# Kernel tuning notes

Hardware: AMD Instinct MI355X
Metric: run time of the kernel (lower is better)

## Reference

```python
import jax, jax.numpy as jnp
import numpy as np


def setup_inputs() -> dict:
    key = jax.random.key(0)
    k1, k2, k3 = jax.random.split(key, 3)
    n_sup, n_qry, d, n_classes = 512, 2097152, 64, 16
    support_features = jax.random.normal(k1, (n_sup, d), dtype=jnp.float32)
    query_features = jax.random.normal(k2, (n_qry, d), dtype=jnp.float32)
    support_labels = jnp.arange(n_sup, dtype=jnp.int64) % n_classes  # every class populated
    query_labels = jax.random.randint(k3, (n_qry,), 0, n_classes, dtype=jnp.int64)
    return {
        "support_features": support_features,
        "query_features": query_features,
        "support_labels": support_labels,
        "query_labels": query_labels,
        "n_classes": n_classes,
        "n_iter": 50,
        "beta": 5,
    }


def _sq_dists(q, q_sq, centroids):
    # squared Euclidean distances [Nq, C]; q_sq precomputed row norms of q
    return q_sq[:, None] - 2.0 * (q @ centroids.T) + jnp.sum(centroids * centroids, axis=-1)[None, :]


def reference(support_features, query_features, support_labels, query_labels, n_classes, n_iter, beta):
    dtype = support_features.dtype
    beta_f = jnp.asarray(beta, dtype)
    # per-class support sums/counts (hard assignments, fixed across iterations)
    oh = jax.nn.one_hot(support_labels, n_classes, dtype=dtype)        # [Ns, C]
    class_counts = jnp.sum(oh, axis=0)                                  # [C]
    sup_sum = oh.T @ support_features                                   # [C, d]
    centroids = sup_sum / class_counts[:, None]                         # class means init

    q_sq = jnp.sum(query_features * query_features, axis=-1)            # [Nq]

    def step(centroids, _):
        d2 = _sq_dists(query_features, q_sq, centroids)                 # [Nq, C]
        w = jax.nn.softmax(-beta_f * d2, axis=-1)                       # soft assignments
        num = sup_sum + w.T @ query_features                            # [C, d]
        den = class_counts + jnp.sum(w, axis=0)                         # [C]
        return num / den[:, None], None

    centroids, _ = jax.lax.scan(step, centroids, None, length=n_iter)

    d2 = _sq_dists(query_features, q_sq, centroids)
    pred = jnp.argmin(d2, axis=-1)
    acc = jnp.mean((pred == query_labels).astype(jnp.float32))
    return acc
```

## Files before the change

### kernel.cpp

```cpp
#include <hip/hip_runtime.h>
#include <stdint.h>

typedef short bf16x8 __attribute__((ext_vector_type(8)));
typedef float f32x4 __attribute__((ext_vector_type(4)));
typedef float f32x2 __attribute__((ext_vector_type(2)));
typedef uint32_t u32x4 __attribute__((ext_vector_type(4)));
typedef uint32_t u32x2 __attribute__((ext_vector_type(2)));
typedef int i32x2 __attribute__((ext_vector_type(2)));
typedef unsigned short u16;
typedef long long i64;

#define ITERS 50
#define BETA_F 5.0f

#define WS_SUPSUM 0
#define WS_COUNTS 1024
#define WS_CENT   1040
#define WS_CSQ    2064
#define WS_ACC    2080
#define WS_CORR   10400
#define WS_Q8_OFF 10432

__device__ __forceinline__ u16 f2bf(float x) {
  union { float f; uint32_t u; } v; v.f = x;
  uint32_t r = (v.u + 0x7FFFu + ((v.u >> 16) & 1u)) >> 16;
  return (u16)r;
}
__device__ __forceinline__ uint32_t fkey(float f) {
  union { float f; uint32_t u; } v; v.f = f;
  return (v.u & 0x80000000u) ? ~v.u : (v.u | 0x80000000u);
}
__device__ __forceinline__ uint32_t pk8(float a, float b, float c, float d) {
  int r = __builtin_amdgcn_cvt_pk_fp8_f32(a, b, 0, false);
  r = __builtin_amdgcn_cvt_pk_fp8_f32(c, d, r, true);
  return (uint32_t)r;
}
__device__ __forceinline__ i64 pack64(uint32_t lo, uint32_t hi) {
  return (i64)(((uint64_t)hi << 32) | (uint64_t)lo);
}
__device__ __forceinline__ void quant_hilo4(float v0, float v1, float v2, float v3,
                                            uint32_t& hi, uint32_t& lo, float& sq) {
  uint32_t h = pk8(v0, v1, v2, v3);
  float h0 = __builtin_amdgcn_cvt_f32_fp8((int)h, 0);
  float h1 = __builtin_amdgcn_cvt_f32_fp8((int)h, 1);
  float h2 = __builtin_amdgcn_cvt_f32_fp8((int)h, 2);
  float h3 = __builtin_amdgcn_cvt_f32_fp8((int)h, 3);
  uint32_t l = pk8(v0 - h0, v1 - h1, v2 - h2, v3 - h3);
  float c0 = h0 + __builtin_amdgcn_cvt_f32_fp8((int)l, 0);
  float c1 = h1 + __builtin_amdgcn_cvt_f32_fp8((int)l, 1);
  float c2 = h2 + __builtin_amdgcn_cvt_f32_fp8((int)l, 2);
  float c3 = h3 + __builtin_amdgcn_cvt_f32_fp8((int)l, 3);
  sq += c0 * c0 + c1 * c1 + c2 * c2 + c3 * c3;
  hi = h; lo = l;
}

__device__ __forceinline__ i32x2 ds_tr8(const uint8_t* p) {
#if defined(__has_builtin)
#if __has_builtin(__builtin_amdgcn_ds_read_tr8_b64)
#define HAVE_TR8 1
#endif
#endif
#ifdef HAVE_TR8
  typedef __attribute__((address_space(3))) i32x2 lds_i32x2;
  return __builtin_amdgcn_ds_read_tr8_b64((lds_i32x2*)p);
#else
  uint32_t off = (uint32_t)(uintptr_t)(__attribute__((address_space(3))) const void*)p;
  i32x2 r;
  asm volatile("ds_read_b64_tr_b8 %0, %1\n\ts_waitcnt lgkmcnt(0)"
               : "=v"(r) : "v"(off) : "memory");
  __builtin_amdgcn_sched_barrier(0);
  return r;
#endif
}

template <int CTRL>
__device__ __forceinline__ float dppf(float x) {
  int i = __builtin_bit_cast(int, x);
  int r = __builtin_amdgcn_update_dpp(i, i, CTRL, 0xF, 0xF, false);
  return __builtin_bit_cast(float, r);
}
template <int CTRL>
__device__ __forceinline__ uint32_t dppu(uint32_t x) {
  int r = __builtin_amdgcn_update_dpp((int)x, (int)x, CTRL, 0xF, 0xF, false);
  return (uint32_t)r;
}
__device__ __forceinline__ float rmax16(float x) {
  x = fmaxf(x, dppf<0xB1>(x));
  x = fmaxf(x, dppf<0x4E>(x));
  x = fmaxf(x, dppf<0x141>(x));
  x = fmaxf(x, dppf<0x140>(x));
  return x;
}
__device__ __forceinline__ float rsum16(float x) {
  x += dppf<0xB1>(x);
  x += dppf<0x4E>(x);
  x += dppf<0x141>(x);
  x += dppf<0x140>(x);
  return x;
}
__device__ __forceinline__ uint32_t rumax16(uint32_t x) {
  uint32_t t;
  t = dppu<0xB1>(x);  x = (t > x) ? t : x;
  t = dppu<0x4E>(x);  x = (t > x) ? t : x;
  t = dppu<0x141>(x); x = (t > x) ? t : x;
  t = dppu<0x140>(x); x = (t > x) ? t : x;
  return x;
}

__global__ __launch_bounds__(1024) void init_kernel(const float* __restrict__ sup,
                                                    const int* __restrict__ slab,
                                                    int NS, float* __restrict__ ws) {
  const int tid = threadIdx.x;
  const int c = tid >> 6, j = tid & 63;
  float s = 0.f; int cnt = 0;
  for (int i = 0; i < NS; ++i) {
    int lbl = slab[i];
    float v = sup[i * 64 + j];
    if (lbl == c) { s += v; cnt++; }
  }
  ws[WS_SUPSUM + tid] = s;
  if (j == 0) ws[WS_COUNTS + c] = (float)cnt;
  ws[WS_CENT + tid] = s / (float)cnt;
  for (int i = tid; i < 8 * 1040; i += 1024) ws[WS_ACC + i] = 0.f;
  if (tid == 0) ws[WS_CORR] = 0.f;
  __syncthreads();
  if (j == 0) {
    float sq = 0.f;
    for (int k = 0; k < 64; ++k) { float v = ws[WS_CENT + c * 64 + k]; sq += v * v; }
    ws[WS_CSQ + c] = sq;
  }
}

template <bool SRC_F8, bool WRC8>
__global__ __launch_bounds__(256, 4) void pass_kernel(const float* __restrict__ qf,
                                                      uint8_t* __restrict__ q8,
                                                      int NQ, float* __restrict__ ws) {
  __shared__ __attribute__((aligned(16))) uint8_t qt8[4][2048];
  __shared__ __attribute__((aligned(16))) uint8_t w8[4][16][32];
  __shared__ float redden[16];

  const int tid = threadIdx.x;
  const int lane = tid & 63;
  const int wv = tid >> 6;
  const int c = lane & 15;
  const int g = lane >> 4;

  const float* cent = ws + WS_CENT;
  const int cb = c * 64 + g * 8;
  uint32_t bh0a, bl0a, bh0b, bl0b, bh1a, bl1a, bh1b, bl1b;
  float csq = 0.f;
  quant_hilo4(cent[cb + 0], cent[cb + 1], cent[cb + 2], cent[cb + 3], bh0a, bl0a, csq);
  quant_hilo4(cent[cb + 4], cent[cb + 5], cent[cb + 6], cent[cb + 7], bh0b, bl0b, csq);
  quant_hilo4(cent[cb + 32], cent[cb + 33], cent[cb + 34], cent[cb + 35], bh1a, bl1a, csq);
  quant_hilo4(cent[cb + 36], cent[cb + 37], cent[cb + 38], cent[cb + 39], bh1b, bl1b, csq);
  csq += __shfl_xor(csq, 16);
  csq += __shfl_xor(csq, 32);
  const i64 bh0 = pack64(bh0a, bh0b), bl0 = pack64(bl0a, bl0b);
  const i64 bh1 = pack64(bh1a, bh1b), bl1 = pack64(bl1a, bl1b);
  const float kcn = -BETA_F * csq;

  f32x4 acc[4] = {};
  float denacc = 0.f;

  uint8_t* qtw = &qt8[wv][0];
  const uint8_t* trb = qtw + c + g * 128;
  uint8_t* w8w = &w8[wv][c][0];
  const int woff = (g >> 1) * 512 + (g & 1) * 8;

  const int wave_id = blockIdx.x * 4 + wv;
  const int nwaves = gridDim.x * 4;
  const int ntiles = NQ >> 5;

  auto LOADQ = [&](int tl, u32x2 (&da)[2], u32x2 (&db)[2]) {
    const int qb0 = tl << 5;
#pragma unroll
    for (int st = 0; st < 2; ++st) {
      const int q = qb0 + st * 16 + c;
      if (SRC_F8) {
        u32x4 v = *(const u32x4*)(q8 + (size_t)q * 64 + g * 16);
        da[st][0] = v[0]; da[st][1] = v[1];
        db[st][0] = v[2]; db[st][1] = v[3];
      } else {
        const float* qr = qf + (size_t)q * 64 + g * 8;
        f32x4 v0 = *(const f32x4*)(qr);
        f32x4 v1 = *(const f32x4*)(qr + 4);
        f32x4 v2 = *(const f32x4*)(qr + 32);
        f32x4 v3 = *(const f32x4*)(qr + 36);
        da[st][0] = pk8(v0[0], v0[1], v0[2], v0[3]);
        da[st][1] = pk8(v1[0], v1[1], v1[2], v1[3]);
        db[st][0] = pk8(v2[0], v2[1], v2[2], v2[3]);
        db[st][1] = pk8(v3[0], v3[1], v3[2], v3[3]);
        if (WRC8) {
          u32x4 o; o[0] = da[st][0]; o[1] = da[st][1]; o[2] = db[st][0]; o[3] = db[st][1];
          *(u32x4*)(q8 + (size_t)q * 64 + g * 16) = o;
        }
      }
    }
  };

  u32x2 qa[2] = {}, qb_[2] = {}, na_[2] = {}, nb_[2] = {};
  int tile = wave_id;
  if (tile < ntiles) LOADQ(tile, qa, qb_);
  for (; tile < ntiles; tile += nwaves) {
    if (tile + nwaves < ntiles) LOADQ(tile + nwaves, na_, nb_);
#pragma unroll
    for (int st = 0; st < 2; ++st) {
      const int row = st * 16 + c;
      *(u32x2*)(qtw + woff + row * 16) = qa[st];
      *(u32x2*)(qtw + woff + row * 16 + 1024) = qb_[st];
      const i64 a0 = __builtin_bit_cast(i64, qa[st]);
      const i64 a1 = __builtin_bit_cast(i64, qb_[st]);
      f32x4 sc4 = {};
      sc4 = __builtin_amdgcn_mfma_f32_16x16x32_fp8_fp8(a0, bh0, sc4, 0, 0, 0);
      sc4 = __builtin_amdgcn_mfma_f32_16x16x32_fp8_fp8(a0, bl0, sc4, 0, 0, 0);
      sc4 = __builtin_amdgcn_mfma_f32_16x16x32_fp8_fp8(a1, bh1, sc4, 0, 0, 0);
      sc4 = __builtin_amdgcn_mfma_f32_16x16x32_fp8_fp8(a1, bl1, sc4, 0, 0, 0);
      float wr[4];
#pragma unroll
      for (int r = 0; r < 4; ++r) {
        float sv = fmaf(sc4[r], 2.0f * BETA_F, kcn);
        float m = rmax16(sv);
        float e = __expf(sv - m);
        float s = rsum16(e);
        wr[r] = e * __builtin_amdgcn_rcpf(s);
      }
      uint32_t w32 = pk8(wr[0], wr[1], wr[2], wr[3]);
      *(uint32_t*)(w8w + st * 16 + g * 4) = w32;
      f32x2 d0 = __builtin_amdgcn_cvt_pk_f32_fp8((int)w32, false);
      f32x2 d1 = __builtin_amdgcn_cvt_pk_f32_fp8((int)w32, true);
      denacc += (d0[0] + d0[1]) + (d1[0] + d1[1]);
    }
    const i64 aw = *(const i64*)(w8w + g * 8);
#pragma unroll
    for (int nt = 0; nt < 4; ++nt) {
      i32x2 bq = ds_tr8(trb + nt * 512);
      acc[nt] = __builtin_amdgcn_mfma_f32_16x16x32_fp8_fp8(
          aw, __builtin_bit_cast(i64, bq), acc[nt], 0, 0, 0);
    }
#pragma unroll
    for (int st = 0; st < 2; ++st) { qa[st] = na_[st]; qb_[st] = nb_[st]; }
  }

  __syncthreads();
  float* red = (float*)&qt8[0][0];
  for (int i = tid; i < 1024; i += 256) red[i] = 0.f;
  if (tid < 16) redden[tid] = 0.f;
  __syncthreads();
#pragma unroll
  for (int nt = 0; nt < 4; ++nt)
#pragma unroll
    for (int r = 0; r < 4; ++r)
      atomicAdd(&red[(g * 4 + r) * 64 + nt * 16 + c], acc[nt][r]);
  atomicAdd(&redden[c], denacc);
  __syncthreads();
  float* accn = ws + WS_ACC + (size_t)(blockIdx.x & 7) * 1040;
  for (int i = tid; i < 1024; i += 256) atomicAdd(&accn[i], red[i]);
  if (tid < 16) atomicAdd(&accn[1024 + tid], redden[tid]);
}

__global__ __launch_bounds__(1024) void update_kernel(float* __restrict__ ws) {
  const int tid = threadIdx.x;
  const int c = tid >> 6;
  float num = ws[WS_SUPSUM + tid];
  float den = ws[WS_COUNTS + c];
#pragma unroll
  for (int rep = 0; rep < 8; ++rep) {
    num += ws[WS_ACC + rep * 1040 + tid];
    den += ws[WS_ACC + rep * 1040 + 1024 + c];
  }
  ws[WS_CENT + tid] = num / den;
  for (int i = tid; i < 8 * 1040; i += 1024) ws[WS_ACC + i] = 0.f;
  __syncthreads();
  if ((tid & 63) == 0) {
    float sq = 0.f;
    for (int k = 0; k < 64; ++k) { float v = ws[WS_CENT + c * 64 + k]; sq += v * v; }
    ws[WS_CSQ + c] = sq;
  }
}

__global__ __launch_bounds__(256, 4) void final_kernel(const float* __restrict__ qf,
                                                       const int* __restrict__ qlab,
                                                       int NQ, float* __restrict__ ws) {
  const int tid = threadIdx.x;
  const int lane = tid & 63;
  const int c = lane & 15;
  const int g = lane >> 4;

  const float* cent = ws + WS_CENT;
  bf16x8 bc0, bc1;
#pragma unroll
  for (int j = 0; j < 8; ++j) {
    bc0[j] = (short)f2bf(cent[c * 64 + g * 8 + j]);
    bc1[j] = (short)f2bf(cent[c * 64 + 32 + g * 8 + j]);
  }
  const float csq = ws[WS_CSQ + c];

  int cnt = 0;
  const int wave_id = blockIdx.x * 4 + (tid >> 6);
  const int nwaves = gridDim.x * 4;
  const int ntiles = NQ >> 4;

  for (int tile = wave_id; tile < ntiles; tile += nwaves) {
    const int qbase = tile << 4;
    const int q = qbase + c;
    const float* qrow = qf + (size_t)q * 64;
    bf16x8 a0, a1;
#pragma unroll
    for (int j = 0; j < 8; ++j) {
      a0[j] = (short)f2bf(qrow[g * 8 + j]);
      a1[j] = (short)f2bf(qrow[32 + g * 8 + j]);
    }
    f32x4 sc = (f32x4){0.f, 0.f, 0.f, 0.f};
    sc = __builtin_amdgcn_mfma_f32_16x16x32_bf16(a0, bc0, sc, 0, 0, 0);
    sc = __builtin_amdgcn_mfma_f32_16x16x32_bf16(a1, bc1, sc, 0, 0, 0);
#pragma unroll
    for (int r = 0; r < 4; ++r) {
      float val = 2.f * sc[r] - csq;
      uint32_t key = (fkey(val) & 0xFFFFFFF0u) | (uint32_t)(15 - c);
      key = rumax16(key);
      int pred = 15 - (int)(key & 15u);
      if (c == 0) cnt += (qlab[qbase + g * 4 + r] == pred) ? 1 : 0;
    }
  }
#pragma unroll
  for (int msk = 1; msk < 64; msk <<= 1) cnt += __shfl_xor(cnt, msk);
  if (lane == 0) atomicAdd(&ws[WS_CORR], (float)cnt);
}

__global__ void finalize_kernel(const float* __restrict__ ws, float* __restrict__ out, float inv) {
  out[0] = ws[WS_CORR] * inv;
}

extern "C" void kernel_launch(void* const* d_in, const int* in_sizes, int n_in,
                              void* d_out, int out_size, void* d_ws, size_t ws_size,
                              hipStream_t stream) {
  const float* sup = (const float*)d_in[0];
  const float* qf  = (const float*)d_in[1];
  const int* slab  = (const int*)d_in[2];
  const int* qlab  = (const int*)d_in[3];
  float* ws = (float*)d_ws;
  float* out = (float*)d_out;
  const int NS = in_sizes[0] / 64;
  const int NQ = in_sizes[1] / 64;
  uint8_t* q8 = (uint8_t*)(ws + WS_Q8_OFF);
  const size_t need = (size_t)WS_Q8_OFF * 4 + (size_t)NQ * 64;
  const bool use_f8 = (ws_size >= need);

  init_kernel<<<1, 1024, 0, stream>>>(sup, slab, NS, ws);
  for (int it = 0; it < ITERS; ++it) {
    if (it == 0) {
      if (use_f8) pass_kernel<false, true><<<2048, 256, 0, stream>>>(qf, q8, NQ, ws);
      else        pass_kernel<false, false><<<2048, 256, 0, stream>>>(qf, q8, NQ, ws);
    } else {
      if (use_f8) pass_kernel<true, false><<<2048, 256, 0, stream>>>(qf, q8, NQ, ws);
      else        pass_kernel<false, false><<<2048, 256, 0, stream>>>(qf, q8, NQ, ws);
    }
    update_kernel<<<1, 1024, 0, stream>>>(ws);
  }
  final_kernel<<<2048, 256, 0, stream>>>(qf, qlab, NQ, ws);
  finalize_kernel<<<1, 1, 0, stream>>>(ws, out, 1.0f / (float)NQ);
}
```

Before: 5.244 ms.

## Replace global atomic accumulation with per-block partials and parallel reduction

Each pass block now writes its class sums and denominators to its own row of a partials buffer instead of doing global atomicAdds into 8 replicated accumulators. The update kernel becomes 16 blocks, one per class, that reduce all partial rows in parallel and compute the centroid norms with shuffles, so accumulators no longer need zeroing. The pass grid is halved to 1024 blocks to keep the partial buffer small. This removes global atomic contention and the single-block update bottleneck, at the cost of extra partial traffic and possibly lower pass occupancy.

After: 7.957 ms. +51.7%, slower.

```diff
diff --git a/kernel.cpp b/kernel.cpp
--- a/kernel.cpp
+++ b/kernel.cpp
@@ -12,14 +12,15 @@
 
 #define ITERS 50
 #define BETA_F 5.0f
+#define NPASS_BLOCKS 1024
 
 #define WS_SUPSUM 0
 #define WS_COUNTS 1024
 #define WS_CENT   1040
 #define WS_CSQ    2064
-#define WS_ACC    2080
 #define WS_CORR   10400
-#define WS_Q8_OFF 10432
+#define WS_PART   10432
+#define WS_Q8_OFF (WS_PART + NPASS_BLOCKS * 1056)
 
 __device__ __forceinline__ u16 f2bf(float x) {
   union { float f; uint32_t u; } v; v.f = x;
@@ -121,7 +122,6 @@
   ws[WS_SUPSUM + tid] = s;
   if (j == 0) ws[WS_COUNTS + c] = (float)cnt;
   ws[WS_CENT + tid] = s / (float)cnt;
-  for (int i = tid; i < 8 * 1040; i += 1024) ws[WS_ACC + i] = 0.f;
   if (tid == 0) ws[WS_CORR] = 0.f;
   __syncthreads();
   if (j == 0) {
@@ -253,28 +253,42 @@
       atomicAdd(&red[(g * 4 + r) * 64 + nt * 16 + c], acc[nt][r]);
   atomicAdd(&redden[c], denacc);
   __syncthreads();
-  float* accn = ws + WS_ACC + (size_t)(blockIdx.x & 7) * 1040;
-  for (int i = tid; i < 1024; i += 256) atomicAdd(&accn[i], red[i]);
-  if (tid < 16) atomicAdd(&accn[1024 + tid], redden[tid]);
-}
-
-__global__ __launch_bounds__(1024) void update_kernel(float* __restrict__ ws) {
-  const int tid = threadIdx.x;
-  const int c = tid >> 6;
-  float num = ws[WS_SUPSUM + tid];
-  float den = ws[WS_COUNTS + c];
-#pragma unroll
-  for (int rep = 0; rep < 8; ++rep) {
-    num += ws[WS_ACC + rep * 1040 + tid];
-    den += ws[WS_ACC + rep * 1040 + 1024 + c];
-  }
-  ws[WS_CENT + tid] = num / den;
-  for (int i = tid; i < 8 * 1040; i += 1024) ws[WS_ACC + i] = 0.f;
-  __syncthreads();
-  if ((tid & 63) == 0) {
-    float sq = 0.f;
-    for (int k = 0; k < 64; ++k) { float v = ws[WS_CENT + c * 64 + k]; sq += v * v; }
-    ws[WS_CSQ + c] = sq;
+  float* prow = ws + WS_PART + (size_t)blockIdx.x * 1056;
+  for (int i = tid; i < 1024; i += 256) prow[i] = red[i];
+  if (tid < 16) prow[1024 + tid] = redden[tid];
+}
+
+__global__ __launch_bounds__(256) void update_kernel(float* __restrict__ ws, int npart) {
+  const int cls = blockIdx.x;
+  const int t = threadIdx.x;
+  const int j = t & 63;
+  const int q4 = t >> 6;
+  const float* base = ws + WS_PART;
+
+  float s = 0.f;
+  for (int b = q4; b < npart; b += 4)
+    s += base[(size_t)b * 1056 + cls * 64 + j];
+
+  float d = 0.f;
+  for (int b = t; b < npart; b += 256)
+    d += base[(size_t)b * 1056 + 1024 + cls];
+#pragma unroll
+  for (int m = 1; m < 64; m <<= 1) d += __shfl_xor(d, m);
+
+  __shared__ float sh[4][64];
+  __shared__ float shd[4];
+  sh[q4][j] = s;
+  if ((t & 63) == 0) shd[t >> 6] = d;
+  __syncthreads();
+  if (t < 64) {
+    float den = shd[0] + shd[1] + shd[2] + shd[3] + ws[WS_COUNTS + cls];
+    float num = sh[0][t] + sh[1][t] + sh[2][t] + sh[3][t] + ws[WS_SUPSUM + cls * 64 + t];
+    float cv = num / den;
+    ws[WS_CENT + cls * 64 + t] = cv;
+    float sq = cv * cv;
+#pragma unroll
+    for (int m = 1; m < 64; m <<= 1) sq += __shfl_xor(sq, m);
+    if (t == 0) ws[WS_CSQ + cls] = sq;
   }
 }
 
@@ -349,13 +363,13 @@
   init_kernel<<<1, 1024, 0, stream>>>(sup, slab, NS, ws);
   for (int it = 0; it < ITERS; ++it) {
     if (it == 0) {
-      if (use_f8) pass_kernel<false, true><<<2048, 256, 0, stream>>>(qf, q8, NQ, ws);
-      else        pass_kernel<false, false><<<2048, 256, 0, stream>>>(qf, q8, NQ, ws);
+      if (use_f8) pass_kernel<false, true><<<NPASS_BLOCKS, 256, 0, stream>>>(qf, q8, NQ, ws);
+      else        pass_kernel<false, false><<<NPASS_BLOCKS, 256, 0, stream>>>(qf, q8, NQ, ws);
     } else {
-      if (use_f8) pass_kernel<true, false><<<2048, 256, 0, stream>>>(qf, q8, NQ, ws);
-      else        pass_kernel<false, false><<<2048, 256, 0, stream>>>(qf, q8, NQ, ws);
-    }
-    update_kernel<<<1, 1024, 0, stream>>>(ws);
+      if (use_f8) pass_kernel<true, false><<<NPASS_BLOCKS, 256, 0, stream>>>(qf, q8, NQ, ws);
+      else        pass_kernel<false, false><<<NPASS_BLOCKS, 256, 0, stream>>>(qf, q8, NQ, ws);
+    }
+    update_kernel<<<16, 256, 0, stream>>>(ws, NPASS_BLOCKS);
   }
   final_kernel<<<2048, 256, 0, stream>>>(qf, qlab, NQ, ws);
   finalize_kernel<<<1, 1, 0, stream>>>(ws, out, 1.0f / (float)NQ);
```
